# Performance work log

Measured on AMD Instinct MI355X. Metric: run time of the kernel, lower is better.

## Reference

```python
import jax, jax.numpy as jnp
import numpy as np

# BERT-base dims; 768 and max_sent_num=64 come from the module/config.
N, S, V, D, L, H, F = 8, 512, 30522, 768, 12, 12, 3072
DH = D // H
MAX_SENT = 64
LN_EPS = 1e-12
SCALE = float(np.sqrt(DH))


def _ln(x, g, b):
    m = jnp.mean(x, axis=-1, keepdims=True)
    v = jnp.mean(jnp.square(x - m), axis=-1, keepdims=True)
    return (x - m) * jax.lax.rsqrt(v + LN_EPS) * g + b


def setup_inputs() -> dict:
    key = jax.random.key(0)
    ks = jax.random.split(key, 10)
    # random token ids in a range avoiding the special ids 102/103
    ids = jax.random.randint(ks[0], (N, S), 999, 30000, dtype=jnp.int32)
    # variable per-doc sentence region -> ragged number of [MASK](103) separators (8..64)
    cutoff = jax.random.randint(ks[1], (N, 1), 64, S + 1)
    pos = jnp.arange(S)[None, :]
    sent_pos = ((pos % 8) == 7) & (pos < cutoff)
    ids = jnp.where(sent_pos, 103, ids)
    ids = ids.at[:, 0].set(102)  # exactly one [SEP]=102 per doc (required by the slice-assign)
    amask = jnp.ones((N, S), dtype=jnp.int32)
    g = lambda k, shape: 0.02 * jax.random.normal(k, shape, dtype=jnp.float32)
    inp = dict(input_ids_bert=ids, attention_mask_bert=amask)
    inp["tok_emb"] = g(ks[2], (V, D))
    inp["pos_emb"] = g(ks[3], (S, D))
    inp["emb_ln_g"] = jnp.ones((D,), jnp.float32)
    inp["emb_ln_b"] = jnp.zeros((D,), jnp.float32)
    inp["Wqkv"] = g(ks[4], (L, D, 3 * D))
    inp["bqkv"] = jnp.zeros((L, 3 * D), jnp.float32)
    inp["Wo"] = g(ks[5], (L, D, D))
    inp["bo"] = jnp.zeros((L, D), jnp.float32)
    inp["ln1_g"] = jnp.ones((L, D), jnp.float32)
    inp["ln1_b"] = jnp.zeros((L, D), jnp.float32)
    inp["W1"] = g(ks[6], (L, D, F))
    inp["b1"] = jnp.zeros((L, F), jnp.float32)
    inp["W2"] = g(ks[7], (L, F, D))
    inp["b2"] = jnp.zeros((L, D), jnp.float32)
    inp["ln2_g"] = jnp.ones((L, D), jnp.float32)
    inp["ln2_b"] = jnp.zeros((L, D), jnp.float32)
    return inp


def _bert(ids, amask, tok_emb, pos_emb, emb_ln_g, emb_ln_b,
          Wqkv, bqkv, Wo, bo, ln1_g, ln1_b, W1, b1, W2, b2, ln2_g, ln2_b):
    x = tok_emb[ids] + pos_emb[None, :, :]            # [N,S,D]
    x = _ln(x, emb_ln_g, emb_ln_b)
    bias = (1.0 - amask[:, None, None, :].astype(x.dtype)) * -1e9  # [N,1,1,S]

    def layer(x, p):
        wqkv, bq, wo, bo_, g1, b1n, w1, b1f, w2, b2f, g2, b2n = p
        qkv = x @ wqkv + bq
        q, k, v = jnp.split(qkv, 3, axis=-1)
        q = q.reshape(N, S, H, DH)
        k = k.reshape(N, S, H, DH)
        v = v.reshape(N, S, H, DH)
        att = jnp.einsum('bqhd,bkhd->bhqk', q, k) / SCALE + bias
        att = jax.nn.softmax(att, axis=-1)
        o = jnp.einsum('bhqk,bkhd->bqhd', att, v).reshape(N, S, D)
        x2 = _ln(x + o @ wo + bo_, g1, b1n)
        h = jax.nn.gelu(x2 @ w1 + b1f, approximate=False)
        return _ln(x2 + h @ w2 + b2f, g2, b2n), None

    x, _ = jax.lax.scan(layer, x, (Wqkv, bqkv, Wo, bo, ln1_g, ln1_b, W1, b1, W2, b2, ln2_g, ln2_b))
    return x


def _gather_scatter(ids, h):
    # Vectorized form of the per-doc python loop:
    #   out[doc, :n_sent] = concat([cls_emb(102), sent_embs(103)])[:-1]
    mask_sent = ids == 103
    mask_cls = ids == 102
    n_cls = mask_cls.sum(axis=1, keepdims=True)              # == 1 per doc
    total_sent = mask_sent.sum(axis=1, keepdims=True)        # ragged count
    rank_sent = jnp.cumsum(mask_sent, axis=1) - 1
    rank_cls = jnp.cumsum(mask_cls, axis=1) - 1
    dest = jnp.where(mask_cls, rank_cls,
                     jnp.where(mask_sent, n_cls + rank_sent, MAX_SENT))
    valid = (mask_cls | mask_sent) & (dest < total_sent) & (dest < MAX_SENT)
    dest_safe = jnp.where(valid, dest, MAX_SENT)             # dump invalid into scratch row
    vals = jnp.where(valid[..., None], h, 0.0)
    out = jnp.zeros((ids.shape[0], MAX_SENT + 1, D), dtype=h.dtype)
    out = out.at[jnp.arange(ids.shape[0])[:, None], dest_safe].set(vals)
    return out[:, :MAX_SENT]


def reference(input_ids_bert, attention_mask_bert, tok_emb, pos_emb, emb_ln_g, emb_ln_b,
              Wqkv, bqkv, Wo, bo, ln1_g, ln1_b, W1, b1, W2, b2, ln2_g, ln2_b):
    h = _bert(input_ids_bert, attention_mask_bert, tok_emb, pos_emb, emb_ln_g, emb_ln_b,
              Wqkv, bqkv, Wo, bo, ln1_g, ln1_b, W1, b1, W2, b2, ln2_g, ln2_b)
    return _gather_scatter(input_ids_bert, h)
```

## Files before the change

kernel.cpp:

```cpp
#include <hip/hip_runtime.h>
#include <hip/hip_bf16.h>

#define DEV static __device__ __forceinline__

using short8 = __attribute__((ext_vector_type(8))) short;
using f32x4 = __attribute__((ext_vector_type(4))) float;

DEV short f2bf(float f) {
  union { float f; unsigned u; } x; x.f = f;
  unsigned r = x.u + 0x7fffu + ((x.u >> 16) & 1u);
  return (short)(r >> 16);
}

DEV float bf2f(short s) {
  union { unsigned u; float f; } x; x.u = ((unsigned)(unsigned short)s) << 16;
  return x.f;
}

DEV void gload16(const void* g, void* lds) {
  __builtin_amdgcn_global_load_lds(
      (const __attribute__((address_space(1))) void*)g,
      (__attribute__((address_space(3))) void*)lds, 16, 0, 0);
}

DEV float erf_fast(float x) {
  float ax = fabsf(x);
  float t = __fdividef(1.f, 1.f + 0.3275911f * ax);
  float y = t * (0.254829592f + t * (-0.284496736f +
            t * (1.421413741f + t * (-1.453152027f + t * 1.061405429f))));
  float r = 1.f - y * __expf(-ax * ax);
  return copysignf(r, x);
}

DEV void swz_grid(int& bx, int& by, int& bz) {
  const int nx = gridDim.x, ny = gridDim.y;
  const int nwg = nx * ny * (int)gridDim.z;
  const int lin = (int)blockIdx.x + nx * ((int)blockIdx.y + ny * (int)blockIdx.z);
  const int cpx = nwg >> 3;
  const int s = (lin & 7) * cpx + (lin >> 3);
  bx = s % nx;
  const int t = s / nx;
  by = t % ny;
  bz = t / ny;
}

DEV void transpose_tile(const float* in, short* out, int K, int N, int tt, int nt,
                        int tid, short (*t)[72]) {
  const int n0 = (tt % nt) * 64, k0 = (tt / nt) * 64;
  #pragma unroll
  for (int p = 0; p < 4; ++p) {
    int r = p * 16 + (tid >> 4), c4 = tid & 15;
    float4 v = *reinterpret_cast<const float4*>(in + (size_t)(k0 + r) * N + n0 + c4 * 4);
    t[r][c4 * 4 + 0] = f2bf(v.x);
    t[r][c4 * 4 + 1] = f2bf(v.y);
    t[r][c4 * 4 + 2] = f2bf(v.z);
    t[r][c4 * 4 + 3] = f2bf(v.w);
  }
  __syncthreads();
  #pragma unroll
  for (int q = 0; q < 2; ++q) {
    int n = tid >> 2, kc = (tid & 3) + q * 4;
    short8 o;
    #pragma unroll
    for (int j = 0; j < 8; ++j) o[j] = t[kc * 8 + j][n];
    *reinterpret_cast<short8*>(out + (size_t)(n0 + n) * K + k0 + kc * 8) = o;
  }
}

__global__ __launch_bounds__(256) void transpose_all_k(
    const float* __restrict__ Wqkv, const float* __restrict__ Wo,
    const float* __restrict__ W1, const float* __restrict__ W2,
    short* __restrict__ wqkvT, short* __restrict__ woT,
    short* __restrict__ w1T, short* __restrict__ w2T)
{
  __shared__ short t[64][72];
  const int b = blockIdx.x, tid = threadIdx.x;
  const float* in; short* out; int K, N, tt, nt;
  if (b < 432)       { in = Wqkv; out = wqkvT; K = 768;  N = 2304; tt = b;        nt = 36; }
  else if (b < 576)  { in = Wo;   out = woT;   K = 768;  N = 768;  tt = b - 432;  nt = 12; }
  else if (b < 1152) { in = W1;   out = w1T;   K = 768;  N = 3072; tt = b - 576;  nt = 48; }
  else               { in = W2;   out = w2T;   K = 3072; N = 768;  tt = b - 1152; nt = 12; }
  transpose_tile(in, out, K, N, tt, nt, tid, t);
}

__global__ __launch_bounds__(256) void transpose12_k(
    const float* __restrict__ Wqkv, const float* __restrict__ Wo,
    const float* __restrict__ W1, const float* __restrict__ W2,
    short* __restrict__ wqkvT, short* __restrict__ woT,
    short* __restrict__ w1T, short* __restrict__ w2T)
{
  __shared__ short t[64][72];
  const int b = blockIdx.x, l = blockIdx.z, tid = threadIdx.x;
  const float* in; short* out; int K, N, tt, nt;
  if (b < 432)       { in = Wqkv + (size_t)l * 768 * 2304; out = wqkvT + (size_t)l * 2304 * 768; K = 768;  N = 2304; tt = b;        nt = 36; }
  else if (b < 576)  { in = Wo   + (size_t)l * 768 * 768;  out = woT   + (size_t)l * 768 * 768;  K = 768;  N = 768;  tt = b - 432;  nt = 12; }
  else if (b < 1152) { in = W1   + (size_t)l * 768 * 3072; out = w1T   + (size_t)l * 3072 * 768; K = 768;  N = 3072; tt = b - 576;  nt = 48; }
  else               { in = W2   + (size_t)l * 3072 * 768; out = w2T   + (size_t)l * 768 * 3072; K = 3072; N = 768;  tt = b - 1152; nt = 12; }
  transpose_tile(in, out, K, N, tt, nt, tid, t);
}

template <int BM, int EPI>
__global__ __launch_bounds__(256) void gemm_bt(
    const short* __restrict__ A, const short* __restrict__ Bt,
    const float* __restrict__ bias, const float* __restrict__ resid,
    void* __restrict__ Cout, int M, int Nn, int K)
{
  constexpr int AW = BM / 64;
  constexpr int MI = BM / 32;
  __shared__ short As[2 * BM * 32];
  __shared__ short Bs[2 * 128 * 32];
  int bx, by, bz;
  swz_grid(bx, by, bz);
  const int tid = threadIdx.x, lane = tid & 63, w = tid >> 6;
  const int wr = w >> 1, wc = w & 1;
  const int l15 = lane & 15, l4 = lane >> 4;
  const int m0 = by * BM, n0 = bx * 128;
  const int crow = lane >> 2, ccol = (lane & 3) * 8;

  f32x4 acc[MI][4] = {};

  for (int k0 = 0; k0 < K; k0 += 64) {
    #pragma unroll
    for (int ks = 0; ks < 2; ++ks) {
      #pragma unroll
      for (int s = 0; s < AW; ++s) {
        int c = w * AW + s;
        gload16(A + (size_t)(m0 + c * 16 + crow) * K + k0 + ks * 32 + ccol,
                &As[ks * BM * 32 + c * 512]);
      }
      #pragma unroll
      for (int s = 0; s < 2; ++s) {
        int c = w * 2 + s;
        gload16(Bt + (size_t)(n0 + c * 16 + crow) * K + k0 + ks * 32 + ccol,
                &Bs[ks * 128 * 32 + c * 512]);
      }
    }
    __syncthreads();

    #pragma unroll
    for (int ks = 0; ks < 2; ++ks) {
      short8 af[MI], bfr[4];
      #pragma unroll
      for (int i = 0; i < MI; ++i)
        af[i] = *reinterpret_cast<const short8*>(
            &As[ks * BM * 32 + (wr * (BM / 2) + i * 16 + l15) * 32 + l4 * 8]);
      #pragma unroll
      for (int j = 0; j < 4; ++j)
        bfr[j] = *reinterpret_cast<const short8*>(
            &Bs[ks * 128 * 32 + (wc * 64 + j * 16 + l15) * 32 + l4 * 8]);
      #pragma unroll
      for (int i = 0; i < MI; ++i)
        #pragma unroll
        for (int j = 0; j < 4; ++j)
          acc[i][j] = __builtin_amdgcn_mfma_f32_16x16x32_bf16(af[i], bfr[j], acc[i][j], 0, 0, 0);
    }
    __syncthreads();
  }

  #pragma unroll
  for (int i = 0; i < MI; ++i) {
    #pragma unroll
    for (int j = 0; j < 4; ++j) {
      #pragma unroll
      for (int r = 0; r < 4; ++r) {
        int row = m0 + wr * (BM / 2) + i * 16 + l4 * 4 + r;
        int col = n0 + wc * 64 + j * 16 + l15;
        float v = acc[i][j][r] + bias[col];
        if constexpr (EPI == 1) v = 0.5f * v * (1.0f + erf_fast(v * 0.70710678118654752f));
        ((short*)Cout)[(size_t)row * Nn + col] = f2bf(v);
      }
    }
  }
}

__global__ __launch_bounds__(256) void gemm_sk(
    const short* __restrict__ A, const short* __restrict__ Bt,
    short* __restrict__ p0, short* __restrict__ p1,
    short* __restrict__ p2, short* __restrict__ p3,
    int M, int Nn, int Kstride, int Klen)
{
  __shared__ short As[2 * 128 * 32];
  __shared__ short Bs[2 * 128 * 32];
  int bx, by, bz;
  swz_grid(bx, by, bz);
  const int tid = threadIdx.x, lane = tid & 63, w = tid >> 6;
  const int wr = w >> 1, wc = w & 1;
  const int l15 = lane & 15, l4 = lane >> 4;
  const int m0 = by * 128, n0 = bx * 128;
  const int koff = bz * Klen;
  const int crow = lane >> 2, ccol = (lane & 3) * 8;

  f32x4 acc[4][4] = {};

  for (int k0 = 0; k0 < Klen; k0 += 64) {
    #pragma unroll
    for (int ks = 0; ks < 2; ++ks) {
      #pragma unroll
      for (int s = 0; s < 2; ++s) {
        int c = w * 2 + s;
        gload16(A + (size_t)(m0 + c * 16 + crow) * Kstride + koff + k0 + ks * 32 + ccol,
                &As[ks * 4096 + c * 512]);
      }
      #pragma unroll
      for (int s = 0; s < 2; ++s) {
        int c = w * 2 + s;
        gload16(Bt + (size_t)(n0 + c * 16 + crow) * Kstride + koff + k0 + ks * 32 + ccol,
                &Bs[ks * 4096 + c * 512]);
      }
    }
    __syncthreads();

    #pragma unroll
    for (int ks = 0; ks < 2; ++ks) {
      short8 af[4], bfr[4];
      #pragma unroll
      for (int i = 0; i < 4; ++i)
        af[i] = *reinterpret_cast<const short8*>(
            &As[ks * 4096 + (wr * 64 + i * 16 + l15) * 32 + l4 * 8]);
      #pragma unroll
      for (int j = 0; j < 4; ++j)
        bfr[j] = *reinterpret_cast<const short8*>(
            &Bs[ks * 4096 + (wc * 64 + j * 16 + l15) * 32 + l4 * 8]);
      #pragma unroll
      for (int i = 0; i < 4; ++i)
        #pragma unroll
        for (int j = 0; j < 4; ++j)
          acc[i][j] = __builtin_amdgcn_mfma_f32_16x16x32_bf16(af[i], bfr[j], acc[i][j], 0, 0, 0);
    }
    __syncthreads();
  }

  short* P = (bz == 0) ? p0 : (bz == 1) ? p1 : (bz == 2) ? p2 : p3;
  #pragma unroll
  for (int i = 0; i < 4; ++i)
    #pragma unroll
    for (int j = 0; j < 4; ++j)
      #pragma unroll
      for (int r = 0; r < 4; ++r) {
        int row = m0 + wr * 64 + i * 16 + l4 * 4 + r;
        int col = n0 + wc * 64 + j * 16 + l15;
        P[(size_t)row * Nn + col] = f2bf(acc[i][j][r]);
      }
}

__global__ __launch_bounds__(256) void attn_k(
    const short* __restrict__ qkv, const int* __restrict__ amask,
    short* __restrict__ out)
{
  __shared__ short Kl[64][72];
  __shared__ short Vt[64][68];
  __shared__ short Pl[4][16][72];
  int bx, by, bz;
  swz_grid(bx, by, bz);
  const int b = bz, h = by, qt = bx;
  const int tid = threadIdx.x, lane = tid & 63, w = tid >> 6;
  const int l15 = lane & 15, l4 = lane >> 4;
  const int tok0 = b * 512;
  const int q0 = qt * 64 + w * 16;

  short8 qf[2];
  #pragma unroll
  for (int kk = 0; kk < 2; ++kk)
    qf[kk] = *reinterpret_cast<const short8*>(
        qkv + (size_t)(tok0 + q0 + l15) * 2304 + h * 64 + kk * 32 + l4 * 8);

  f32x4 oacc[4] = {};
  float mrow[4], lrow[4];
  #pragma unroll
  for (int r = 0; r < 4; ++r) { mrow[r] = -1e30f; lrow[r] = 0.f; }

  for (int kt0 = 0; kt0 < 512; kt0 += 64) {
    #pragma unroll
    for (int i = 0; i < 2; ++i) {
      int c = tid + i * 256;
      int r = c >> 3, dc = c & 7;
      short8 v = *reinterpret_cast<const short8*>(
          qkv + (size_t)(tok0 + kt0 + r) * 2304 + 768 + h * 64 + dc * 8);
      *reinterpret_cast<short8*>(&Kl[r][dc * 8]) = v;
    }
    #pragma unroll
    for (int i = 0; i < 2; ++i) {
      int c = tid + i * 256;
      int r = c >> 3, dc = c & 7;
      short8 v = *reinterpret_cast<const short8*>(
          qkv + (size_t)(tok0 + kt0 + r) * 2304 + 1536 + h * 64 + dc * 8);
      #pragma unroll
      for (int j = 0; j < 8; ++j) Vt[dc * 8 + j][r] = v[j];
    }
    __syncthreads();

    f32x4 sacc[4] = {};
    #pragma unroll
    for (int t = 0; t < 4; ++t) {
      #pragma unroll
      for (int kk = 0; kk < 2; ++kk) {
        short8 kf = *reinterpret_cast<const short8*>(&Kl[t * 16 + l15][kk * 32 + l4 * 8]);
        sacc[t] = __builtin_amdgcn_mfma_f32_16x16x32_bf16(qf[kk], kf, sacc[t], 0, 0, 0);
      }
    }
    float p[4][4];
    #pragma unroll
    for (int t = 0; t < 4; ++t) {
      int ktok = kt0 + t * 16 + l15;
      float biasv = amask[b * 512 + ktok] ? 0.f : -1e9f;
      #pragma unroll
      for (int r = 0; r < 4; ++r) p[t][r] = sacc[t][r] * 0.125f + biasv;
    }
    #pragma unroll
    for (int r = 0; r < 4; ++r) {
      float mx = fmaxf(fmaxf(p[0][r], p[1][r]), fmaxf(p[2][r], p[3][r]));
      #pragma unroll
      for (int s = 1; s <= 8; s <<= 1) mx = fmaxf(mx, __shfl_xor(mx, s, 64));
      float mnew = fmaxf(mrow[r], mx);
      float alpha = __expf(mrow[r] - mnew);
      mrow[r] = mnew;
      float sum = 0.f;
      #pragma unroll
      for (int t = 0; t < 4; ++t) { p[t][r] = __expf(p[t][r] - mnew); sum += p[t][r]; }
      #pragma unroll
      for (int s = 1; s <= 8; s <<= 1) sum += __shfl_xor(sum, s, 64);
      lrow[r] = lrow[r] * alpha + sum;
      #pragma unroll
      for (int t = 0; t < 4; ++t) oacc[t][r] *= alpha;
    }
    #pragma unroll
    for (int t = 0; t < 4; ++t)
      #pragma unroll
      for (int r = 0; r < 4; ++r)
        Pl[w][l4 * 4 + r][t * 16 + l15] = f2bf(p[t][r]);
    #pragma unroll
    for (int kk = 0; kk < 2; ++kk) {
      short8 pf = *reinterpret_cast<const short8*>(&Pl[w][l15][kk * 32 + l4 * 8]);
      #pragma unroll
      for (int t = 0; t < 4; ++t) {
        const unsigned* vp = reinterpret_cast<const unsigned*>(&Vt[t * 16 + l15][0]);
        union { short8 s; unsigned u[4]; } vu;
        #pragma unroll
        for (int w2 = 0; w2 < 4; ++w2) vu.u[w2] = vp[kk * 16 + l4 * 4 + w2];
        oacc[t] = __builtin_amdgcn_mfma_f32_16x16x32_bf16(pf, vu.s, oacc[t], 0, 0, 0);
      }
    }
    __syncthreads();
  }

  #pragma unroll
  for (int t = 0; t < 4; ++t)
    #pragma unroll
    for (int r = 0; r < 4; ++r) {
      int tok = tok0 + q0 + l4 * 4 + r;
      int dh = t * 16 + l15;
      out[(size_t)tok * 768 + h * 64 + dh] = f2bf(oacc[t][r] / lrow[r]);
    }
}

__global__ __launch_bounds__(256) void ln2_k(
    const short* __restrict__ p0, const short* __restrict__ p1,
    const short* __restrict__ p2, const short* __restrict__ p3,
    const float* __restrict__ bias, const float* __restrict__ resid,
    const float* __restrict__ g, const float* __restrict__ be,
    float* __restrict__ xf, short* __restrict__ xb)
{
  const int t = blockIdx.x, tid = threadIdx.x;
  const size_t base = (size_t)t * 768;
  float v[3], s = 0.f, ss = 0.f;
  #pragma unroll
  for (int i = 0; i < 3; ++i) {
    int c = tid + i * 256;
    v[i] = (bf2f(p0[base + c]) + bf2f(p1[base + c]))
         + (bf2f(p2[base + c]) + bf2f(p3[base + c]))
         + bias[c] + resid[base + c];
    s += v[i]; ss += v[i] * v[i];
  }
  __shared__ float red[4][2];
  #pragma unroll
  for (int m = 1; m <= 32; m <<= 1) { s += __shfl_xor(s, m, 64); ss += __shfl_xor(ss, m, 64); }
  int w = tid >> 6;
  if ((tid & 63) == 0) { red[w][0] = s; red[w][1] = ss; }
  __syncthreads();
  s = red[0][0] + red[1][0] + red[2][0] + red[3][0];
  ss = red[0][1] + red[1][1] + red[2][1] + red[3][1];
  float mean = s * (1.f / 768.f);
  float var = ss * (1.f / 768.f) - mean * mean;
  float rs = rsqrtf(var + 1e-12f);
  #pragma unroll
  for (int i = 0; i < 3; ++i) {
    int c = tid + i * 256;
    float o = (v[i] - mean) * rs * g[c] + be[c];
    xf[base + c] = o;
    xb[base + c] = f2bf(o);
  }
}

__global__ __launch_bounds__(256) void embed_ln_k(
    const int* __restrict__ ids, const float* __restrict__ tok_emb,
    const float* __restrict__ pos_emb, const float* __restrict__ g,
    const float* __restrict__ be, float* __restrict__ xf, short* __restrict__ xb)
{
  const int t = blockIdx.x, tid = threadIdx.x;
  const int id = ids[t], sp = t & 511;
  float v[3], s = 0.f, ss = 0.f;
  #pragma unroll
  for (int i = 0; i < 3; ++i) {
    int c = tid + i * 256;
    v[i] = tok_emb[(size_t)id * 768 + c] + pos_emb[(size_t)sp * 768 + c];
    s += v[i]; ss += v[i] * v[i];
  }
  __shared__ float red[4][2];
  #pragma unroll
  for (int m = 1; m <= 32; m <<= 1) { s += __shfl_xor(s, m, 64); ss += __shfl_xor(ss, m, 64); }
  int w = tid >> 6;
  if ((tid & 63) == 0) { red[w][0] = s; red[w][1] = ss; }
  __syncthreads();
  s = red[0][0] + red[1][0] + red[2][0] + red[3][0];
  ss = red[0][1] + red[1][1] + red[2][1] + red[3][1];
  float mean = s * (1.f / 768.f);
  float var = ss * (1.f / 768.f) - mean * mean;
  float rs = rsqrtf(var + 1e-12f);
  #pragma unroll
  for (int i = 0; i < 3; ++i) {
    int c = tid + i * 256;
    float o = (v[i] - mean) * rs * g[c] + be[c];
    xf[(size_t)t * 768 + c] = o;
    xb[(size_t)t * 768 + c] = f2bf(o);
  }
}

__global__ __launch_bounds__(512) void gather_k(
    const int* __restrict__ ids, const float* __restrict__ x, float* __restrict__ out)
{
  const int doc = blockIdx.x, tid = threadIdx.x;
  const int lane = tid & 63, w = tid >> 6;
  __shared__ int src[64];
  __shared__ int wave_sent[8];
  __shared__ int cls_pos;
  if (tid < 64) src[tid] = -1;
  if (tid == 0) cls_pos = 0x7fffffff;
  __syncthreads();

  const int id = ids[doc * 512 + tid];
  const bool is_sent = (id == 103);
  const unsigned long long m = __ballot(is_sent);
  if (lane == 0) wave_sent[w] = __popcll(m);
  if (id == 102) atomicMin(&cls_pos, tid);
  __syncthreads();

  int total = 0, prefix = 0;
  #pragma unroll
  for (int i = 0; i < 8; ++i) {
    int c = wave_sent[i];
    if (i < w) prefix += c;
    total += c;
  }
  if (is_sent) {
    unsigned long long lt = lane ? (~0ULL >> (64 - lane)) : 0ULL;
    int d = 1 + prefix + __popcll(m & lt);
    if (d < total && d < 64) src[d] = tid;
  }
  if (tid == 0 && total > 0 && cls_pos != 0x7fffffff) src[0] = cls_pos;
  __syncthreads();

  for (int i = tid; i < 64 * 192; i += 512) {
    int row = i / 192, c4 = i - row * 192;
    int sp = src[row];
    float4 v = make_float4(0.f, 0.f, 0.f, 0.f);
    if (sp >= 0)
      v = reinterpret_cast<const float4*>(x + (size_t)(doc * 512 + sp) * 768)[c4];
    reinterpret_cast<float4*>(out + (size_t)doc * 64 * 768)[i] = v;
  }
}

extern "C" void kernel_launch(void* const* d_in, const int* in_sizes, int n_in,
                              void* d_out, int out_size, void* d_ws, size_t ws_size,
                              hipStream_t stream)
{
  const int* ids = (const int*)d_in[0];
  const int* am = (const int*)d_in[1];
  const float* tok_emb = (const float*)d_in[2];
  const float* pos_emb = (const float*)d_in[3];
  const float* eg = (const float*)d_in[4];
  const float* eb = (const float*)d_in[5];
  const float* Wqkv = (const float*)d_in[6];
  const float* bqkv = (const float*)d_in[7];
  const float* Wo = (const float*)d_in[8];
  const float* bo = (const float*)d_in[9];
  const float* g1 = (const float*)d_in[10];
  const float* b1n = (const float*)d_in[11];
  const float* W1 = (const float*)d_in[12];
  const float* b1f = (const float*)d_in[13];
  const float* W2 = (const float*)d_in[14];
  const float* b2f = (const float*)d_in[15];
  const float* g2 = (const float*)d_in[16];
  const float* b2n = (const float*)d_in[17];

  char* ws = (char*)d_ws;
  float* x_f   = (float*)(ws);
  short* x_b   = (short*)(ws + 12582912);
  float* x2_f  = (float*)(ws + 18874368);
  short* x2_b  = (short*)(ws + 31457280);
  short* pp0   = (short*)(ws + 37748736);
  short* pp1   = (short*)(ws + 37748736 + 6291456);
  short* qkv   = (short*)(ws + 50331648);
  short* pp2   = (short*)(ws + 50331648);
  short* pp3   = (short*)(ws + 50331648 + 6291456);
  short* attn  = (short*)(ws + 69206016);
  short* hb    = (short*)(ws + 75497472);
  const size_t WQ = 2304ull * 768, WO = 768ull * 768, W1S = 3072ull * 768, W2S = 768ull * 3072;
  const size_t NEED_ALL = 100663296ull + 12ull * (WQ + WO + W1S + W2S) * 2ull;
  const bool big = ws_size >= NEED_ALL;

  short* wqkvT = (short*)(ws + 100663296);
  short* woT, *w1T, *w2T;
  if (big) {
    woT = wqkvT + 12 * WQ;
    w1T = woT + 12 * WO;
    w2T = w1T + 12 * W1S;
  } else {
    woT = (short*)(ws + 104202240);
    w1T = (short*)(ws + 105381888);
    w2T = (short*)(ws + 110100480);
  }

  embed_ln_k<<<4096, 256, 0, stream>>>(ids, tok_emb, pos_emb, eg, eb, x_f, x_b);

  if (big)
    transpose12_k<<<dim3(1728, 1, 12), 256, 0, stream>>>(
        Wqkv, Wo, W1, W2, wqkvT, woT, w1T, w2T);

  for (int l = 0; l < 12; ++l) {
    short *wq, *wo, *w1, *w2;
    if (big) {
      wq = wqkvT + l * WQ; wo = woT + l * WO; w1 = w1T + l * W1S; w2 = w2T + l * W2S;
    } else {
      transpose_all_k<<<1728, 256, 0, stream>>>(
          Wqkv + (size_t)l * 768 * 2304, Wo + (size_t)l * 768 * 768,
          W1 + (size_t)l * 768 * 3072, W2 + (size_t)l * 3072 * 768,
          wqkvT, woT, w1T, w2T);
      wq = wqkvT; wo = woT; w1 = w1T; w2 = w2T;
    }

    gemm_bt<128, 0><<<dim3(18, 32), 256, 0, stream>>>(
        x_b, wq, bqkv + (size_t)l * 2304, nullptr, qkv, 4096, 2304, 768);
    attn_k<<<dim3(8, 12, 8), 256, 0, stream>>>(qkv, am, attn);

    gemm_sk<<<dim3(6, 32, 4), 256, 0, stream>>>(
        attn, wo, pp0, pp1, pp2, pp3, 4096, 768, 768, 192);
    ln2_k<<<4096, 256, 0, stream>>>(
        pp0, pp1, pp2, pp3, bo + (size_t)l * 768, x_f,
        g1 + (size_t)l * 768, b1n + (size_t)l * 768, x2_f, x2_b);

    gemm_bt<128, 1><<<dim3(24, 32), 256, 0, stream>>>(
        x2_b, w1, b1f + (size_t)l * 3072, nullptr, hb, 4096, 3072, 768);

    gemm_sk<<<dim3(6, 32, 4), 256, 0, stream>>>(
        hb, w2, pp0, pp1, pp2, pp3, 4096, 768, 3072, 768);
    ln2_k<<<4096, 256, 0, stream>>>(
        pp0, pp1, pp2, pp3, b2f + (size_t)l * 768, x2_f,
        g2 + (size_t)l * 768, b2n + (size_t)l * 768, x_f, x_b);
  }

  gather_k<<<8, 512, 0, stream>>>(ids, x_f, (float*)d_out);
}
```

Baseline: 2.240 ms.

## Use one wave per row for layernorm, drop grid swizzle, repad transpose LDS

The layernorm kernels (embedding and residual) now give each token row to a single 64-lane wave instead of a 256-thread block. Loads and stores are vectorised to two elements per lane, and the shared-memory reduction and barrier are gone. The XCD-aware grid swizzle is removed from the GEMM and attention kernels, so they use plain blockIdx mapping. The transpose LDS padding changes from 72 to 76 columns. Dropping the swizzle may hurt L2 locality across chiplets.

```diff
diff --git a/kernel.cpp b/kernel.cpp
--- a/kernel.cpp
+++ b/kernel.cpp
@@ -15,6 +15,10 @@
 DEV float bf2f(short s) {
   union { unsigned u; float f; } x; x.u = ((unsigned)(unsigned short)s) << 16;
   return x.f;
+}
+
+DEV unsigned pack2bf(float a, float b) {
+  return (unsigned)(unsigned short)f2bf(a) | ((unsigned)(unsigned short)f2bf(b) << 16);
 }
 
 DEV void gload16(const void* g, void* lds) {
@@ -32,20 +36,8 @@
   return copysignf(r, x);
 }
 
-DEV void swz_grid(int& bx, int& by, int& bz) {
-  const int nx = gridDim.x, ny = gridDim.y;
-  const int nwg = nx * ny * (int)gridDim.z;
-  const int lin = (int)blockIdx.x + nx * ((int)blockIdx.y + ny * (int)blockIdx.z);
-  const int cpx = nwg >> 3;
-  const int s = (lin & 7) * cpx + (lin >> 3);
-  bx = s % nx;
-  const int t = s / nx;
-  by = t % ny;
-  bz = t / ny;
-}
-
 DEV void transpose_tile(const float* in, short* out, int K, int N, int tt, int nt,
-                        int tid, short (*t)[72]) {
+                        int tid, short (*t)[76]) {
   const int n0 = (tt % nt) * 64, k0 = (tt / nt) * 64;
   #pragma unroll
   for (int p = 0; p < 4; ++p) {
@@ -73,7 +65,7 @@
     short* __restrict__ wqkvT, short* __restrict__ woT,
     short* __restrict__ w1T, short* __restrict__ w2T)
 {
-  __shared__ short t[64][72];
+  __shared__ short t[64][76];
   const int b = blockIdx.x, tid = threadIdx.x;
   const float* in; short* out; int K, N, tt, nt;
   if (b < 432)       { in = Wqkv; out = wqkvT; K = 768;  N = 2304; tt = b;        nt = 36; }
@@ -89,7 +81,7 @@
     short* __restrict__ wqkvT, short* __restrict__ woT,
     short* __restrict__ w1T, short* __restrict__ w2T)
 {
-  __shared__ short t[64][72];
+  __shared__ short t[64][76];
   const int b = blockIdx.x, l = blockIdx.z, tid = threadIdx.x;
   const float* in; short* out; int K, N, tt, nt;
   if (b < 432)       { in = Wqkv + (size_t)l * 768 * 2304; out = wqkvT + (size_t)l * 2304 * 768; K = 768;  N = 2304; tt = b;        nt = 36; }
@@ -109,12 +101,10 @@
   constexpr int MI = BM / 32;
   __shared__ short As[2 * BM * 32];
   __shared__ short Bs[2 * 128 * 32];
-  int bx, by, bz;
-  swz_grid(bx, by, bz);
   const int tid = threadIdx.x, lane = tid & 63, w = tid >> 6;
   const int wr = w >> 1, wc = w & 1;
   const int l15 = lane & 15, l4 = lane >> 4;
-  const int m0 = by * BM, n0 = bx * 128;
+  const int m0 = blockIdx.y * BM, n0 = blockIdx.x * 128;
   const int crow = lane >> 2, ccol = (lane & 3) * 8;
 
   f32x4 acc[MI][4] = {};
@@ -181,13 +171,11 @@
 {
   __shared__ short As[2 * 128 * 32];
   __shared__ short Bs[2 * 128 * 32];
-  int bx, by, bz;
-  swz_grid(bx, by, bz);
   const int tid = threadIdx.x, lane = tid & 63, w = tid >> 6;
   const int wr = w >> 1, wc = w & 1;
   const int l15 = lane & 15, l4 = lane >> 4;
-  const int m0 = by * 128, n0 = bx * 128;
-  const int koff = bz * Klen;
+  const int m0 = blockIdx.y * 128, n0 = blockIdx.x * 128;
+  const int koff = blockIdx.z * Klen;
   const int crow = lane >> 2, ccol = (lane & 3) * 8;
 
   f32x4 acc[4][4] = {};
@@ -230,7 +218,7 @@
     __syncthreads();
   }
 
-  short* P = (bz == 0) ? p0 : (bz == 1) ? p1 : (bz == 2) ? p2 : p3;
+  short* P = (blockIdx.z == 0) ? p0 : (blockIdx.z == 1) ? p1 : (blockIdx.z == 2) ? p2 : p3;
   #pragma unroll
   for (int i = 0; i < 4; ++i)
     #pragma unroll
@@ -250,9 +238,7 @@
   __shared__ short Kl[64][72];
   __shared__ short Vt[64][68];
   __shared__ short Pl[4][16][72];
-  int bx, by, bz;
-  swz_grid(bx, by, bz);
-  const int b = bz, h = by, qt = bx;
+  const int b = blockIdx.z, h = blockIdx.y, qt = blockIdx.x;
   const int tid = threadIdx.x, lane = tid & 63, w = tid >> 6;
   const int l15 = lane & 15, l4 = lane >> 4;
   const int tok0 = b * 512;
@@ -360,34 +346,41 @@
     const float* __restrict__ g, const float* __restrict__ be,
     float* __restrict__ xf, short* __restrict__ xb)
 {
-  const int t = blockIdx.x, tid = threadIdx.x;
+  const int w = threadIdx.x >> 6, lane = threadIdx.x & 63;
+  const int t = blockIdx.x * 4 + w;
   const size_t base = (size_t)t * 768;
-  float v[3], s = 0.f, ss = 0.f;
-  #pragma unroll
-  for (int i = 0; i < 3; ++i) {
-    int c = tid + i * 256;
-    v[i] = (bf2f(p0[base + c]) + bf2f(p1[base + c]))
-         + (bf2f(p2[base + c]) + bf2f(p3[base + c]))
-         + bias[c] + resid[base + c];
-    s += v[i]; ss += v[i] * v[i];
-  }
-  __shared__ float red[4][2];
+  float2 v[6];
+  float s = 0.f, ss = 0.f;
+  #pragma unroll
+  for (int e = 0; e < 6; ++e) {
+    int c = e * 128 + lane * 2;
+    unsigned a0 = *reinterpret_cast<const unsigned*>(p0 + base + c);
+    unsigned a1 = *reinterpret_cast<const unsigned*>(p1 + base + c);
+    unsigned a2 = *reinterpret_cast<const unsigned*>(p2 + base + c);
+    unsigned a3 = *reinterpret_cast<const unsigned*>(p3 + base + c);
+    float2 r = *reinterpret_cast<const float2*>(resid + base + c);
+    float2 bb = *reinterpret_cast<const float2*>(bias + c);
+    float vx = (bf2f((short)a0) + bf2f((short)a1))
+             + (bf2f((short)a2) + bf2f((short)a3)) + bb.x + r.x;
+    float vy = (bf2f((short)(a0 >> 16)) + bf2f((short)(a1 >> 16)))
+             + (bf2f((short)(a2 >> 16)) + bf2f((short)(a3 >> 16))) + bb.y + r.y;
+    v[e].x = vx; v[e].y = vy;
+    s += vx + vy; ss += vx * vx + vy * vy;
+  }
   #pragma unroll
   for (int m = 1; m <= 32; m <<= 1) { s += __shfl_xor(s, m, 64); ss += __shfl_xor(ss, m, 64); }
-  int w = tid >> 6;
-  if ((tid & 63) == 0) { red[w][0] = s; red[w][1] = ss; }
-  __syncthreads();
-  s = red[0][0] + red[1][0] + red[2][0] + red[3][0];
-  ss = red[0][1] + red[1][1] + red[2][1] + red[3][1];
   float mean = s * (1.f / 768.f);
   float var = ss * (1.f / 768.f) - mean * mean;
   float rs = rsqrtf(var + 1e-12f);
   #pragma unroll
-  for (int i = 0; i < 3; ++i) {
-    int c = tid + i * 256;
-    float o = (v[i] - mean) * rs * g[c] + be[c];
-    xf[base + c] = o;
-    xb[base + c] = f2bf(o);
+  for (int e = 0; e < 6; ++e) {
+    int c = e * 128 + lane * 2;
+    float2 gg = *reinterpret_cast<const float2*>(g + c);
+    float2 bn = *reinterpret_cast<const float2*>(be + c);
+    float ox = (v[e].x - mean) * rs * gg.x + bn.x;
+    float oy = (v[e].y - mean) * rs * gg.y + bn.y;
+    *reinterpret_cast<float2*>(xf + base + c) = make_float2(ox, oy);
+    *reinterpret_cast<unsigned*>(xb + base + c) = pack2bf(ox, oy);
   }
 }
 
@@ -396,32 +389,35 @@
     const float* __restrict__ pos_emb, const float* __restrict__ g,
     const float* __restrict__ be, float* __restrict__ xf, short* __restrict__ xb)
 {
-  const int t = blockIdx.x, tid = threadIdx.x;
+  const int w = threadIdx.x >> 6, lane = threadIdx.x & 63;
+  const int t = blockIdx.x * 4 + w;
+  const size_t base = (size_t)t * 768;
   const int id = ids[t], sp = t & 511;
-  float v[3], s = 0.f, ss = 0.f;
-  #pragma unroll
-  for (int i = 0; i < 3; ++i) {
-    int c = tid + i * 256;
-    v[i] = tok_emb[(size_t)id * 768 + c] + pos_emb[(size_t)sp * 768 + c];
-    s += v[i]; ss += v[i] * v[i];
-  }
-  __shared__ float red[4][2];
+  float2 v[6];
+  float s = 0.f, ss = 0.f;
+  #pragma unroll
+  for (int e = 0; e < 6; ++e) {
+    int c = e * 128 + lane * 2;
+    float2 te = *reinterpret_cast<const float2*>(tok_emb + (size_t)id * 768 + c);
+    float2 pe = *reinterpret_cast<const float2*>(pos_emb + (size_t)sp * 768 + c);
+    float vx = te.x + pe.x, vy = te.y + pe.y;
+    v[e].x = vx; v[e].y = vy;
+    s += vx + vy; ss += vx * vx + vy * vy;
+  }
   #pragma unroll
   for (int m = 1; m <= 32; m <<= 1) { s += __shfl_xor(s, m, 64); ss += __shfl_xor(ss, m, 64); }
-  int w = tid >> 6;
-  if ((tid & 63) == 0) { red[w][0] = s; red[w][1] = ss; }
-  __syncthreads();
-  s = red[0][0] + red[1][0] + red[2][0] + red[3][0];
-  ss = red[0][1] + red[1][1] + red[2][1] + red[3][1];
   float mean = s * (1.f / 768.f);
   float var = ss * (1.f / 768.f) - mean * mean;
   float rs = rsqrtf(var + 1e-12f);
   #pragma unroll
-  for (int i = 0; i < 3; ++i) {
-    int c = tid + i * 256;
-    float o = (v[i] - mean) * rs * g[c] + be[c];
-    xf[(size_t)t * 768 + c] = o;
-    xb[(size_t)t * 768 + c] = f2bf(o);
+  for (int e = 0; e < 6; ++e) {
+    int c = e * 128 + lane * 2;
+    float2 gg = *reinterpret_cast<const float2*>(g + c);
+    float2 bn = *reinterpret_cast<const float2*>(be + c);
+    float ox = (v[e].x - mean) * rs * gg.x + bn.x;
+    float oy = (v[e].y - mean) * rs * gg.y + bn.y;
+    *reinterpret_cast<float2*>(xf + base + c) = make_float2(ox, oy);
+    *reinterpret_cast<unsigned*>(xb + base + c) = pack2bf(ox, oy);
   }
 }
 
@@ -520,7 +516,7 @@
     w2T = (short*)(ws + 110100480);
   }
 
-  embed_ln_k<<<4096, 256, 0, stream>>>(ids, tok_emb, pos_emb, eg, eb, x_f, x_b);
+  embed_ln_k<<<1024, 256, 0, stream>>>(ids, tok_emb, pos_emb, eg, eb, x_f, x_b);
 
   if (big)
     transpose12_k<<<dim3(1728, 1, 12), 256, 0, stream>>>(
@@ -544,7 +540,7 @@
 
     gemm_sk<<<dim3(6, 32, 4), 256, 0, stream>>>(
         attn, wo, pp0, pp1, pp2, pp3, 4096, 768, 768, 192);
-    ln2_k<<<4096, 256, 0, stream>>>(
+    ln2_k<<<1024, 256, 0, stream>>>(
         pp0, pp1, pp2, pp3, bo + (size_t)l * 768, x_f,
         g1 + (size_t)l * 768, b1n + (size_t)l * 768, x2_f, x2_b);
 
@@ -553,7 +549,7 @@
 
     gemm_sk<<<dim3(6, 32, 4), 256, 0, stream>>>(
         hb, w2, pp0, pp1, pp2, pp3, 4096, 768, 3072, 768);
-    ln2_k<<<4096, 256, 0, stream>>>(
+    ln2_k<<<1024, 256, 0, stream>>>(
         pp0, pp1, pp2, pp3, b2f + (size_t)l * 768, x2_f,
         g2 + (size_t)l * 768, b2n + (size_t)l * 768, x_f, x_b);
   }
```

Result: slower. 2.346 ms (+4.7%).
